# Kernel tuning notes

Measured on AMD Instinct MI355X. Metric: run time of the kernel, lower is better.

The kernel has to match this reference:

```python
import jax, jax.numpy as jnp
import numpy as np

N = 8192
E = 131072
IN_DIM = 3000
HID = 512      # gcn1 out = HID // 2 = 256
OUT = 64
EPS = 1e-12


def gcn_conv(x, W, b, src, dst, n):
    """PyG GCNConv: add self-loops, symmetric norm, gather-matmul-scatter."""
    xw = x @ W                                   # [n, out]
    loop = jnp.arange(n, dtype=src.dtype)
    s = jnp.concatenate([src, loop])             # source j
    d = jnp.concatenate([dst, loop])             # target i
    deg = jax.ops.segment_sum(jnp.ones(s.shape[0], dtype=xw.dtype), d, num_segments=n)
    dinv = deg ** -0.5                           # deg >= 1 due to self-loops
    norm = dinv[s] * dinv[d]                     # [E+n]
    out = jax.ops.segment_sum(norm[:, None] * xw[s], d, num_segments=n)
    return out + b


def avg_readout(emb, mask):
    vsum = mask @ emb                            # [N, h]
    row_sum = jnp.sum(mask, axis=1, keepdims=True)
    g = vsum / row_sum
    nrm = jnp.maximum(jnp.linalg.norm(g, axis=1, keepdims=True), EPS)
    return g / nrm                               # F.normalize(p=2, dim=1)


def bilinear(h, c, Wd, bd):
    # nn.Bilinear(n_h, n_h, 1): out[n,o] = sum_ij h[n,i] Wd[o,i,j] c[n,j] + bd[o]
    return jnp.einsum('ni,oij,nj->no', h, Wd, c) + bd


def setup_inputs() -> dict:
    key = jax.random.key(0)
    k1, k2, k3, k4, k5, k6, k7 = jax.random.split(key, 7)
    gene_data = jax.random.normal(k1, (N, IN_DIM), dtype=jnp.float32)
    # sparse binary neighborhood mask (~16 neighbors/row) + self so row sums > 0
    mask = (jax.random.uniform(k2, (N, N)) < (16.0 / N)).astype(jnp.float32)
    mask = jnp.maximum(mask, jnp.eye(N, dtype=jnp.float32))
    spatial_edge_index = jax.random.randint(k3, (2, E), 0, N, dtype=jnp.int64)
    perm = jax.random.permutation(k4, N).astype(jnp.int64)
    h1 = HID // 2
    W1 = jax.random.normal(k5, (IN_DIM, h1), dtype=jnp.float32) / np.sqrt(IN_DIM)
    b1 = jnp.zeros((h1,), dtype=jnp.float32)
    W2 = jax.random.normal(k6, (h1, OUT), dtype=jnp.float32) / np.sqrt(h1)
    b2 = jnp.zeros((OUT,), dtype=jnp.float32)
    Wd = jax.random.normal(k7, (1, OUT, OUT), dtype=jnp.float32) / np.sqrt(OUT)
    bd = jnp.zeros((1,), dtype=jnp.float32)
    return {"gene_data": gene_data, "mask": mask, "W1": W1, "b1": b1,
            "W2": W2, "b2": b2, "Wd": Wd, "bd": bd,
            "spatial_edge_index": spatial_edge_index, "perm": perm}


def reference(gene_data, mask, W1, b1, W2, b2, Wd, bd, spatial_edge_index, perm):
    src, dst = spatial_edge_index[0], spatial_edge_index[1]
    n = gene_data.shape[0]
    x1 = gene_data
    x1_c = gene_data[perm]                       # permuted (corrupted) graph
    # dropout inactive (eval mode, p=0.0)
    x1 = jax.nn.relu(gcn_conv(x1, W1, b1, src, dst, n))
    x1_c = jax.nn.relu(gcn_conv(x1_c, W1, b1, src, dst, n))
    x1 = jax.nn.relu(gcn_conv(x1, W2, b2, src, dst, n))
    x1_c = jax.nn.relu(gcn_conv(x1_c, W2, b2, src, dst, n))
    g1 = jax.nn.sigmoid(avg_readout(x1, mask))
    g1_c = jax.nn.sigmoid(avg_readout(x1_c, mask))
    ret1 = jnp.concatenate([bilinear(x1, g1, Wd, bd), bilinear(x1_c, g1, Wd, bd)], axis=1)
    ret1_c = jnp.concatenate([bilinear(x1_c, g1_c, Wd, bd), bilinear(x1, g1_c, Wd, bd)], axis=1)
    return (x1, ret1, ret1_c)
```

## Files before the change

### kernel.cpp

```cpp
#include <hip/hip_runtime.h>
#include <hip/hip_bf16.h>

#define NN 8192
#define NMASK 8191
#define IND 3000
#define INDP 3008
#define H1 256
#define OUTD 64

#define GB 512
#define SB 2048
#define PB 544

typedef __bf16 bf16x8 __attribute__((ext_vector_type(8)));
typedef float floatx4 __attribute__((ext_vector_type(4)));

typedef const __attribute__((address_space(1))) void GV;
typedef __attribute__((address_space(3))) void LV;

__device__ __forceinline__ unsigned short f2b(float f) {
    __hip_bfloat16 h = __float2bfloat16(f);
    unsigned short u;
    __builtin_memcpy(&u, &h, 2);
    return u;
}

__device__ __forceinline__ floatx4 b4f(const __hip_bfloat16* p) {
    ushort4 u = *reinterpret_cast<const ushort4*>(p);
    floatx4 r;
    r[0] = __uint_as_float((unsigned)u.x << 16);
    r[1] = __uint_as_float((unsigned)u.y << 16);
    r[2] = __uint_as_float((unsigned)u.z << 16);
    r[3] = __uint_as_float((unsigned)u.w << 16);
    return r;
}


__global__ void k_probe(float code, float* out) {
    if (threadIdx.x == 0 && blockIdx.x == 0) out[0] = code;
}


__global__ void k_pre(const unsigned* __restrict__ eraw, const unsigned* __restrict__ praw,
                      int* __restrict__ flags,
                      const float* __restrict__ W1, const float* __restrict__ W2,
                      __hip_bfloat16* __restrict__ W1t, __hip_bfloat16* __restrict__ W2t) {
    int b = blockIdx.x;
    int t = threadIdx.x;
    if (b < 2) {
        const unsigned* r = (b == 0) ? eraw : praw;
        __shared__ int c;
        if (t == 0) c = 0;
        __syncthreads();
        int z = 0;
        for (int k = t; k < 2048; k += 256)
            if (r[2 * k + 1] == 0u) z++;
        atomicAdd(&c, z);
        __syncthreads();
        if (t == 0) flags[b] = (c > 1024) ? 1 : 0;
    } else if (b < 4) {
        int idx = (b - 2) * 256 + t;
#pragma unroll
        for (int u = 0; u < 4; ++u) {
            int k = idx * 4 + u;
            int c = k >> 3;
            int r = 3000 + (k & 7);
            W1t[(size_t)c * INDP + r] = __float2bfloat16(0.f);
        }
    } else {
        int idx = (b - 4) * 256 + t;
        if (idx < IND * H1) {
            int r = idx / H1, c = idx % H1;
            W1t[(size_t)c * INDP + r] = __float2bfloat16(W1[idx]);
        } else {
            int j = idx - IND * H1;
            if (j < H1 * OUTD) {
                int r = j / OUTD, c = j % OUTD;
                W2t[(size_t)c * H1 + r] = __float2bfloat16(W2[j]);
            }
        }
    }
}


__device__ __forceinline__ void gemm1_body(char* smem, int blk,
                                           const float* __restrict__ A,
                                           const __hip_bfloat16* __restrict__ Bt,
                                           unsigned short* __restrict__ C) {
    unsigned short* As = (unsigned short*)smem;
    unsigned short* Bs = As + 64 * 72;
    int t = threadIdx.x;
    int n0 = (blk & 3) * 64;
    int m0 = (blk >> 2) * 64;
    int lane = t & 63;
    int w = t >> 6;
    int srow = t >> 2;
    int schunk = (t & 3) * 16;
    const float* Arow = A + (size_t)(m0 + srow) * IND + schunk;
    const unsigned short* Brow = (const unsigned short*)Bt + (size_t)(n0 + srow) * INDP + schunk;

    floatx4 acc0 = {0.f, 0.f, 0.f, 0.f}, acc1 = acc0, acc2 = acc0, acc3 = acc0;
    int msub = w * 16;
    int arow = msub + (lane & 15);
    int koff = (lane >> 4) * 8;
    int nlo = lane & 15;

    float4 pa0, pa1, pa2, pa3;
    uint4 pb0, pb1;
    auto load_tile = [&](int k0) {
        float4 z4 = make_float4(0.f, 0.f, 0.f, 0.f);
        uint4 zu = make_uint4(0u, 0u, 0u, 0u);
        pa0 = z4; pa1 = z4; pa2 = z4; pa3 = z4; pb0 = zu; pb1 = zu;
        int kk = k0 + schunk;
        if (kk < IND) {
            const float* ap = Arow + k0;
            pa0 = *reinterpret_cast<const float4*>(ap);
            pa1 = *reinterpret_cast<const float4*>(ap + 4);
            pb0 = *reinterpret_cast<const uint4*>(Brow + k0);
        }
        if (kk + 8 < IND) {
            const float* ap = Arow + k0 + 8;
            pa2 = *reinterpret_cast<const float4*>(ap);
            pa3 = *reinterpret_cast<const float4*>(ap + 4);
            pb1 = *reinterpret_cast<const uint4*>(Brow + k0 + 8);
        }
    };
    load_tile(0);
    for (int k0 = 0; k0 < IND; k0 += 64) {
        uint4 av0, av1, bv0 = pb0, bv1 = pb1;
        {
            unsigned short t8[8] = {f2b(pa0.x), f2b(pa0.y), f2b(pa0.z), f2b(pa0.w),
                                    f2b(pa1.x), f2b(pa1.y), f2b(pa1.z), f2b(pa1.w)};
            __builtin_memcpy(&av0, t8, 16);
        }
        {
            unsigned short t8[8] = {f2b(pa2.x), f2b(pa2.y), f2b(pa2.z), f2b(pa2.w),
                                    f2b(pa3.x), f2b(pa3.y), f2b(pa3.z), f2b(pa3.w)};
            __builtin_memcpy(&av1, t8, 16);
        }
        __syncthreads();
        *reinterpret_cast<uint4*>(&As[srow * 72 + schunk]) = av0;
        *reinterpret_cast<uint4*>(&As[srow * 72 + schunk + 8]) = av1;
        *reinterpret_cast<uint4*>(&Bs[srow * 72 + schunk]) = bv0;
        *reinterpret_cast<uint4*>(&Bs[srow * 72 + schunk + 8]) = bv1;
        __syncthreads();
        if (k0 + 64 < IND) load_tile(k0 + 64);
#pragma unroll
        for (int ks = 0; ks < 64; ks += 32) {
            bf16x8 af = *reinterpret_cast<const bf16x8*>(&As[arow * 72 + ks + koff]);
            bf16x8 b0 = *reinterpret_cast<const bf16x8*>(&Bs[(0 + nlo) * 72 + ks + koff]);
            bf16x8 b1 = *reinterpret_cast<const bf16x8*>(&Bs[(16 + nlo) * 72 + ks + koff]);
            bf16x8 b2 = *reinterpret_cast<const bf16x8*>(&Bs[(32 + nlo) * 72 + ks + koff]);
            bf16x8 b3 = *reinterpret_cast<const bf16x8*>(&Bs[(48 + nlo) * 72 + ks + koff]);
            acc0 = __builtin_amdgcn_mfma_f32_16x16x32_bf16(af, b0, acc0, 0, 0, 0);
            acc1 = __builtin_amdgcn_mfma_f32_16x16x32_bf16(af, b1, acc1, 0, 0, 0);
            acc2 = __builtin_amdgcn_mfma_f32_16x16x32_bf16(af, b2, acc2, 0, 0, 0);
            acc3 = __builtin_amdgcn_mfma_f32_16x16x32_bf16(af, b3, acc3, 0, 0, 0);
        }
    }
    int crow = msub + (lane >> 4) * 4;
    int ccol = lane & 15;
    floatx4 accs[4] = {acc0, acc1, acc2, acc3};
#pragma unroll
    for (int j = 0; j < 4; ++j) {
#pragma unroll
        for (int r = 0; r < 4; ++r) {
            C[(size_t)(m0 + crow + r) * H1 + (n0 + j * 16 + ccol)] = f2b(accs[j][r]);
        }
    }
}

__device__ __forceinline__ void scan_body(char* smem, int blk,
                                          const float* __restrict__ mask,
                                          uint2* __restrict__ ents_g,
                                          float* __restrict__ rsum,
                                          int* __restrict__ rcnt, int n) {
    float (*ring)[4][512] = reinterpret_cast<float (*)[4][512]>(smem);
    int lane = threadIdx.x & 63;
    int w = threadIdx.x >> 6;
    int row = blk * 4 + w;
    const float* mrow = mask + (size_t)row * n;
    uint2* erow = ents_g + ((size_t)row << 6);

    auto issue = [&](int c) {
        int slot = c & 3;
        const float* g0 = mrow + c * 512 + lane * 4;
        __builtin_amdgcn_global_load_lds((GV*)g0, (LV*)&ring[w][slot][0], 16, 0, 0);
        __builtin_amdgcn_global_load_lds((GV*)(g0 + 256), (LV*)&ring[w][slot][256], 16, 0, 0);
    };
    issue(0);
    issue(1);
    issue(2);

    int base = 0;
    float rs = 0.f;
    unsigned long long below = (lane == 63) ? ~0ull >> 1 : (1ull << lane) - 1;
    for (int k = 0; k < 16; ++k) {
        if (k < 13) {
            issue(k + 3);
            asm volatile("s_waitcnt vmcnt(6)" ::: "memory");
        } else if (k == 13) {
            asm volatile("s_waitcnt vmcnt(4)" ::: "memory");
        } else if (k == 14) {
            asm volatile("s_waitcnt vmcnt(2)" ::: "memory");
        } else {
            asm volatile("s_waitcnt vmcnt(0)" ::: "memory");
        }
        int slot = k & 3;
        floatx4 q0 = *reinterpret_cast<floatx4*>(&ring[w][slot][lane * 4]);
        floatx4 q1 = *reinterpret_cast<floatx4*>(&ring[w][slot][256 + lane * 4]);
        int cb = k * 512 + lane * 4;
#pragma unroll
        for (int u = 0; u < 4; ++u) {
            float v = q0[u];
            unsigned long long bal = __ballot(v != 0.f);
            if (v != 0.f) {
                int r = base + __popcll(bal & below);
                if (r < 64) erow[r] = make_uint2((unsigned)(cb + u), __float_as_uint(v));
                rs += v;
            }
            base += __popcll(bal);
        }
#pragma unroll
        for (int u = 0; u < 4; ++u) {
            float v = q1[u];
            unsigned long long bal = __ballot(v != 0.f);
            if (v != 0.f) {
                int r = base + __popcll(bal & below);
                if (r < 64) erow[r] = make_uint2((unsigned)(cb + 256 + u), __float_as_uint(v));
                rs += v;
            }
            base += __popcll(bal);
        }
    }
#pragma unroll
    for (int off = 32; off; off >>= 1) rs += __shfl_xor(rs, off);
    if (lane == 0) {
        rsum[row] = rs;
        rcnt[row] = min(base, 64);
    }
}

__device__ __forceinline__ void prep_body(int idx,
                                          const unsigned* __restrict__ eraw,
                                          const unsigned* __restrict__ praw,
                                          const int* __restrict__ flags,
                                          int* __restrict__ perm32,
                                          int* __restrict__ cnt,
                                          int* __restrict__ adj, int E, int n) {
    if (idx < E) {
        int f = flags[0];
        unsigned s = f ? eraw[2 * (size_t)idx] : eraw[idx];
        unsigned d = f ? eraw[2 * (size_t)(E + idx)] : eraw[E + idx];
        int si = (int)(s & (unsigned)NMASK);
        int di = (int)(d & (unsigned)NMASK);
        int p = atomicAdd(&cnt[di], 1);
        if (p < 64) adj[(di << 6) | p] = si;
    } else {
        int j = idx - E;
        if (j < n) {
            unsigned v = flags[1] ? praw[2 * (size_t)j] : praw[j];
            perm32[j] = (int)(v & (unsigned)NMASK);
        }
    }
}

__global__ __launch_bounds__(256) void k_mega(const float* __restrict__ gene,
                                              const __hip_bfloat16* __restrict__ W1t,
                                              unsigned short* __restrict__ xw1b,
                                              const float* __restrict__ mask,
                                              uint2* __restrict__ ents_g,
                                              float* __restrict__ rsum,
                                              int* __restrict__ rcnt,
                                              const unsigned* __restrict__ eraw,
                                              const unsigned* __restrict__ praw,
                                              const int* __restrict__ flags,
                                              int* __restrict__ perm32,
                                              int* __restrict__ cnt,
                                              int* __restrict__ adj, int E, int n) {
    __shared__ __align__(16) char smem[32768];
    int b = blockIdx.x;
    if (b < GB) {
        gemm1_body(smem, b, gene, W1t, xw1b);
    } else if (b < GB + SB) {
        scan_body(smem, b - GB, mask, ents_g, rsum, rcnt, n);
    } else {
        prep_body((b - GB - SB) * 256 + threadIdx.x, eraw, praw, flags,
                  perm32, cnt, adj, E, n);
    }
}


__global__ __launch_bounds__(256) void k_agg1(const __hip_bfloat16* __restrict__ xw1,
                                              const int* __restrict__ cnt,
                                              const int* __restrict__ adj,
                                              const int* __restrict__ perm,
                                              const float* __restrict__ b1,
                                              __hip_bfloat16* __restrict__ h_all, int n) {
    int lane = threadIdx.x & 63;
    int i = blockIdx.x * 4 + (threadIdx.x >> 6);
    int ci = cnt[i];
    float di = rsqrtf((float)(1 + ci));
    int pi = perm[i];
    float sw = di * di;
    int c4 = lane * 4;
    floatx4 acc = sw * b4f(xw1 + (size_t)i * H1 + c4);
    floatx4 accc = sw * b4f(xw1 + (size_t)pi * H1 + c4);
    int e = min(ci, 64);
    const int* arow = adj + ((size_t)i << 6);
#pragma unroll 4
    for (int t = 0; t < e; ++t) {
        int j = arow[t];
        float wv = di * rsqrtf((float)(1 + cnt[j]));
        int pj = perm[j];
        acc += wv * b4f(xw1 + (size_t)j * H1 + c4);
        accc += wv * b4f(xw1 + (size_t)pj * H1 + c4);
    }
    floatx4 b4 = *reinterpret_cast<const floatx4*>(b1 + c4);
    ushort4 h0, h1;
    h0.x = f2b(fmaxf(acc[0] + b4[0], 0.f));
    h0.y = f2b(fmaxf(acc[1] + b4[1], 0.f));
    h0.z = f2b(fmaxf(acc[2] + b4[2], 0.f));
    h0.w = f2b(fmaxf(acc[3] + b4[3], 0.f));
    h1.x = f2b(fmaxf(accc[0] + b4[0], 0.f));
    h1.y = f2b(fmaxf(accc[1] + b4[1], 0.f));
    h1.z = f2b(fmaxf(accc[2] + b4[2], 0.f));
    h1.w = f2b(fmaxf(accc[3] + b4[3], 0.f));
    *reinterpret_cast<ushort4*>(h_all + (size_t)i * H1 + c4) = h0;
    *reinterpret_cast<ushort4*>(h_all + (size_t)(n + i) * H1 + c4) = h1;
}


__global__ __launch_bounds__(256) void k_gemm2(const __hip_bfloat16* __restrict__ A,
                                               const __hip_bfloat16* __restrict__ Bt,
                                               float* __restrict__ C,
                                               int M, int N, int K) {
    __shared__ __align__(16) unsigned short As[64 * 40];
    __shared__ __align__(16) unsigned short Bs[64 * 40];
    int t = threadIdx.x;
    int m0 = blockIdx.x * 64;
    int n0 = blockIdx.y * 64;
    int lane = t & 63;
    int w = t >> 6;
    int srow = t >> 2;
    int schunk = (t & 3) * 8;
    size_t aoff = (size_t)(m0 + srow) * K + schunk;
    const unsigned short* Brow = (const unsigned short*)Bt + (size_t)(n0 + srow) * K + schunk;

    floatx4 acc0 = {0.f, 0.f, 0.f, 0.f}, acc1 = acc0, acc2 = acc0, acc3 = acc0;
    int msub = w * 16;
    int arow = msub + (lane & 15);
    int koff = (lane >> 4) * 8;
    int nlo = lane & 15;

    uint4 pa = *reinterpret_cast<const uint4*>((const unsigned short*)A + aoff);
    uint4 pb = *reinterpret_cast<const uint4*>(Brow);
    for (int k0 = 0; k0 < K; k0 += 32) {
        uint4 av = pa, bv = pb;
        __syncthreads();
        *reinterpret_cast<uint4*>(&As[srow * 40 + schunk]) = av;
        *reinterpret_cast<uint4*>(&Bs[srow * 40 + schunk]) = bv;
        __syncthreads();
        if (k0 + 32 < K) {
            pa = *reinterpret_cast<const uint4*>((const unsigned short*)A + aoff + k0 + 32);
            pb = *reinterpret_cast<const uint4*>(Brow + k0 + 32);
        }
        bf16x8 af = *reinterpret_cast<const bf16x8*>(&As[arow * 40 + koff]);
        bf16x8 bf0 = *reinterpret_cast<const bf16x8*>(&Bs[(0 + nlo) * 40 + koff]);
        bf16x8 bf1 = *reinterpret_cast<const bf16x8*>(&Bs[(16 + nlo) * 40 + koff]);
        bf16x8 bf2 = *reinterpret_cast<const bf16x8*>(&Bs[(32 + nlo) * 40 + koff]);
        bf16x8 bf3 = *reinterpret_cast<const bf16x8*>(&Bs[(48 + nlo) * 40 + koff]);
        acc0 = __builtin_amdgcn_mfma_f32_16x16x32_bf16(af, bf0, acc0, 0, 0, 0);
        acc1 = __builtin_amdgcn_mfma_f32_16x16x32_bf16(af, bf1, acc1, 0, 0, 0);
        acc2 = __builtin_amdgcn_mfma_f32_16x16x32_bf16(af, bf2, acc2, 0, 0, 0);
        acc3 = __builtin_amdgcn_mfma_f32_16x16x32_bf16(af, bf3, acc3, 0, 0, 0);
    }
    int crow = msub + (lane >> 4) * 4;
    int ccol = lane & 15;
    floatx4 accs[4] = {acc0, acc1, acc2, acc3};
#pragma unroll
    for (int j = 0; j < 4; ++j) {
#pragma unroll
        for (int r = 0; r < 4; ++r) {
            C[(size_t)(m0 + crow + r) * N + (n0 + j * 16 + ccol)] = accs[j][r];
        }
    }
}


__global__ __launch_bounds__(256) void k_agg2(const float* __restrict__ hw_all,
                                              const int* __restrict__ cnt,
                                              const int* __restrict__ adj,
                                              const float* __restrict__ b2,
                                              float* __restrict__ x1_all,
                                              float* __restrict__ out_x1, int n) {
    int lane = threadIdx.x & 63;
    int i = blockIdx.x * 4 + (threadIdx.x >> 6);
    int ci = cnt[i];
    float di = rsqrtf((float)(1 + ci));
    float sw = di * di;
    float acc = sw * hw_all[(size_t)i * OUTD + lane];
    float accc = sw * hw_all[(size_t)(n + i) * OUTD + lane];
    int e = min(ci, 64);
    const int* arow = adj + ((size_t)i << 6);
#pragma unroll 4
    for (int t = 0; t < e; ++t) {
        int j = arow[t];
        float wv = di * rsqrtf((float)(1 + cnt[j]));
        acc += wv * hw_all[(size_t)j * OUTD + lane];
        accc += wv * hw_all[(size_t)(n + j) * OUTD + lane];
    }
    float b = b2[lane];
    float v = fmaxf(acc + b, 0.f);
    float vc = fmaxf(accc + b, 0.f);
    x1_all[(size_t)i * OUTD + lane] = v;
    x1_all[(size_t)(n + i) * OUTD + lane] = vc;
    out_x1[(size_t)i * OUTD + lane] = v;
}


__global__ __launch_bounds__(256) void k_finish(const float* __restrict__ x1_all,
                                                const uint2* __restrict__ ents_g,
                                                const float* __restrict__ rsum,
                                                const int* __restrict__ rcnt,
                                                const float* __restrict__ Wd,
                                                const float* __restrict__ bd,
                                                float* __restrict__ ret1,
                                                float* __restrict__ ret1c, int n) {
    int lane = threadIdx.x & 63;
    int w = threadIdx.x >> 6;
    int row = blockIdx.x * 4 + w;
    int cnt = rcnt[row];
    float rs = rsum[row];
    const uint2* erow = ents_g + ((size_t)row << 6);
    float acc = 0.f, accc = 0.f;
#pragma unroll 2
    for (int e = 0; e < cnt; ++e) {
        uint2 ent = erow[e];
        float m = __uint_as_float(ent.y);
        int j = (int)ent.x;
        acc += m * x1_all[(size_t)j * OUTD + lane];
        accc += m * x1_all[(size_t)(n + j) * OUTD + lane];
    }
    float rst = fmaxf(rs, 1e-20f);
    float g = acc / rst;
    float gc = accc / rst;
    float s1 = g * g, s2 = gc * gc;
#pragma unroll
    for (int off = 32; off; off >>= 1) {
        s1 += __shfl_xor(s1, off);
        s2 += __shfl_xor(s2, off);
    }
    float gn = g / fmaxf(sqrtf(s1), 1e-12f);
    float gnc = gc / fmaxf(sqrtf(s2), 1e-12f);
    float gsig = 1.f / (1.f + __expf(-gn));
    float gcsig = 1.f / (1.f + __expf(-gnc));
    float tg = 0.f, tgc = 0.f;
    const float* wrow = Wd + lane * 64;
#pragma unroll 8
    for (int j = 0; j < 64; ++j) {
        float gj = __shfl(gsig, j);
        float gcj = __shfl(gcsig, j);
        float wv = wrow[j];
        tg += wv * gj;
        tgc += wv * gcj;
    }
    float x = x1_all[(size_t)row * OUTD + lane];
    float xc = x1_all[(size_t)(n + row) * OUTD + lane];
    float r0 = x * tg, r1 = xc * tg, r2 = xc * tgc, r3 = x * tgc;
#pragma unroll
    for (int off = 32; off; off >>= 1) {
        r0 += __shfl_down(r0, off);
        r1 += __shfl_down(r1, off);
        r2 += __shfl_down(r2, off);
        r3 += __shfl_down(r3, off);
    }
    if (lane == 0) {
        float b = bd[0];
        ret1[(size_t)row * 2 + 0] = r0 + b;
        ret1[(size_t)row * 2 + 1] = r1 + b;
        ret1c[(size_t)row * 2 + 0] = r2 + b;
        ret1c[(size_t)row * 2 + 1] = r3 + b;
    }
}


extern "C" void kernel_launch(void* const* d_in, const int* in_sizes, int n_in,
                              void* d_out, int out_size, void* d_ws, size_t ws_size,
                              hipStream_t stream) {
    const float* gene = (const float*)d_in[0];
    const float* mask = (const float*)d_in[1];
    const float* W1 = (const float*)d_in[2];
    const float* b1 = (const float*)d_in[3];
    const float* W2 = (const float*)d_in[4];
    const float* b2 = (const float*)d_in[5];
    const float* Wd = (const float*)d_in[6];
    const float* bd = (const float*)d_in[7];
    const unsigned* eidx_raw = (const unsigned*)d_in[8];
    const unsigned* perm_raw = (const unsigned*)d_in[9];
    const int n = NN;
    const int E = in_sizes[8] / 2;

    char* base = (char*)d_ws;
    char* p = base;
    auto alloc = [&](size_t bytes) -> char* {
        char* r = p;
        p += (bytes + 255) & ~(size_t)255;
        return r;
    };
    int* flags = (int*)alloc(256);
    int* cnt = (int*)alloc((size_t)n * 4);
    int* adj = (int*)alloc((size_t)n * 64 * 4);
    int* perm32 = (int*)alloc((size_t)n * 4);
    uint2* ents_g = (uint2*)alloc((size_t)n * 64 * 8);
    float* rsum = (float*)alloc((size_t)n * 4);
    int* rcnt = (int*)alloc((size_t)n * 4);
    __hip_bfloat16* W2t = (__hip_bfloat16*)alloc((size_t)H1 * OUTD * 2);
    __hip_bfloat16* W1t = (__hip_bfloat16*)alloc((size_t)INDP * H1 * 2);
    __hip_bfloat16* xw1b = (__hip_bfloat16*)alloc((size_t)n * H1 * 2);
    __hip_bfloat16* h_all = (__hip_bfloat16*)alloc((size_t)2 * n * H1 * 2);
    size_t need = (size_t)(p - base);
    float* hw_all = (float*)xw1b;
    float* x1_all = (float*)h_all;

    float* out_x1 = (float*)d_out;
    float* out_ret1 = out_x1 + (size_t)n * OUTD;
    float* out_ret1c = out_ret1 + (size_t)n * 2;

    if (ws_size < need) {
        k_probe<<<1, 64, 0, stream>>>(1000.f + (float)(ws_size >> 20), out_x1);
        return;
    }

    hipMemsetAsync(cnt, 0, (size_t)n * 4, stream);

    k_pre<<<4 + (IND * H1 + H1 * OUTD + 255) / 256, 256, 0, stream>>>(
        eidx_raw, perm_raw, flags, W1, W2, W1t, W2t);

    k_mega<<<GB + SB + PB, 256, 0, stream>>>(gene, W1t, (unsigned short*)xw1b,
                                             mask, ents_g, rsum, rcnt,
                                             eidx_raw, perm_raw, flags,
                                             perm32, cnt, adj, E, n);

    k_agg1<<<n / 4, 256, 0, stream>>>(xw1b, cnt, adj, perm32, b1, h_all, n);

    k_gemm2<<<dim3(2 * n / 64, OUTD / 64), 256, 0, stream>>>(h_all, W2t, hw_all, 2 * n, OUTD, H1);

    k_agg2<<<n / 4, 256, 0, stream>>>(hw_all, cnt, adj, b2, x1_all, out_x1, n);

    k_finish<<<n / 4, 256, 0, stream>>>(x1_all, ents_g, rsum, rcnt, Wd, bd,
                                        out_ret1, out_ret1c, n);
}
```

Baseline: 545.4 us.

## Scan mask with grid-strided chunks and atomic compaction instead of per-row LDS ring

The mask scan no longer assigns one full row to each wave streamed through an LDS ring via global_load_lds. Each wave now processes 16 grid-strided 512-element chunks, loaded straight into registers with a two-deep register prefetch. Nonzeros go into a small per-wave LDS buffer and are then scattered to per-row entry lists using atomic slot counters, and row sums are also built with atomics. rcnt and rsum sit next to cnt so a single memset clears all three. This spreads the memory traffic more evenly and cuts LDS use, at the cost of atomics and nondeterministic entry order. A wave silently drops any nonzeros beyond 56, which is safe only while the mask stays sparse.

```diff
diff --git a/kernel.cpp b/kernel.cpp
--- a/kernel.cpp
+++ b/kernel.cpp
@@ -11,12 +11,10 @@
 #define GB 512
 #define SB 2048
 #define PB 544
+#define SW (SB * 4)
 
 typedef __bf16 bf16x8 __attribute__((ext_vector_type(8)));
 typedef float floatx4 __attribute__((ext_vector_type(4)));
-
-typedef const __attribute__((address_space(1))) void GV;
-typedef __attribute__((address_space(3))) void LV;
 
 __device__ __forceinline__ unsigned short f2b(float f) {
     __hip_bfloat16 h = __float2bfloat16(f);
@@ -175,69 +173,55 @@
                                           uint2* __restrict__ ents_g,
                                           float* __restrict__ rsum,
                                           int* __restrict__ rcnt, int n) {
-    float (*ring)[4][512] = reinterpret_cast<float (*)[4][512]>(smem);
+    uint2 (*ebuf)[56] = reinterpret_cast<uint2 (*)[56]>(smem);
     int lane = threadIdx.x & 63;
     int w = threadIdx.x >> 6;
-    int row = blk * 4 + w;
-    const float* mrow = mask + (size_t)row * n;
-    uint2* erow = ents_g + ((size_t)row << 6);
-
-    auto issue = [&](int c) {
-        int slot = c & 3;
-        const float* g0 = mrow + c * 512 + lane * 4;
-        __builtin_amdgcn_global_load_lds((GV*)g0, (LV*)&ring[w][slot][0], 16, 0, 0);
-        __builtin_amdgcn_global_load_lds((GV*)(g0 + 256), (LV*)&ring[w][slot][256], 16, 0, 0);
+    int gw = blk * 4 + w;
+    unsigned long long below = (lane == 63) ? ~0ull >> 1 : (1ull << lane) - 1;
+
+    auto cptr = [&](int t) {
+        return mask + (((size_t)(gw + t * SW)) << 9) + lane * 8;
     };
-    issue(0);
-    issue(1);
-    issue(2);
+    floatx4 pa0 = *reinterpret_cast<const floatx4*>(cptr(0));
+    floatx4 pa1 = *reinterpret_cast<const floatx4*>(cptr(0) + 4);
+    floatx4 pb0 = *reinterpret_cast<const floatx4*>(cptr(1));
+    floatx4 pb1 = *reinterpret_cast<const floatx4*>(cptr(1) + 4);
 
     int base = 0;
-    float rs = 0.f;
-    unsigned long long below = (lane == 63) ? ~0ull >> 1 : (1ull << lane) - 1;
-    for (int k = 0; k < 16; ++k) {
-        if (k < 13) {
-            issue(k + 3);
-            asm volatile("s_waitcnt vmcnt(6)" ::: "memory");
-        } else if (k == 13) {
-            asm volatile("s_waitcnt vmcnt(4)" ::: "memory");
-        } else if (k == 14) {
-            asm volatile("s_waitcnt vmcnt(2)" ::: "memory");
-        } else {
-            asm volatile("s_waitcnt vmcnt(0)" ::: "memory");
-        }
-        int slot = k & 3;
-        floatx4 q0 = *reinterpret_cast<floatx4*>(&ring[w][slot][lane * 4]);
-        floatx4 q1 = *reinterpret_cast<floatx4*>(&ring[w][slot][256 + lane * 4]);
-        int cb = k * 512 + lane * 4;
-#pragma unroll
-        for (int u = 0; u < 4; ++u) {
-            float v = q0[u];
+    for (int t = 0; t < 16; ++t) {
+        floatx4 c0 = pa0, c1 = pa1;
+        pa0 = pb0; pa1 = pb1;
+        if (t + 2 < 16) {
+            pb0 = *reinterpret_cast<const floatx4*>(cptr(t + 2));
+            pb1 = *reinterpret_cast<const floatx4*>(cptr(t + 2) + 4);
+        }
+        int c = gw + t * SW;
+        int row = c >> 4;
+        int cb = (c & 15) * 512 + lane * 8;
+        float lsum = 0.f;
+        float va[8] = {c0[0], c0[1], c0[2], c0[3], c1[0], c1[1], c1[2], c1[3]};
+#pragma unroll
+        for (int u = 0; u < 8; ++u) {
+            float v = va[u];
             unsigned long long bal = __ballot(v != 0.f);
             if (v != 0.f) {
                 int r = base + __popcll(bal & below);
-                if (r < 64) erow[r] = make_uint2((unsigned)(cb + u), __float_as_uint(v));
-                rs += v;
+                if (r < 56)
+                    ebuf[w][r] = make_uint2(((unsigned)row << 13) | (unsigned)(cb + u),
+                                            __float_as_uint(v));
+                lsum += v;
             }
             base += __popcll(bal);
         }
-#pragma unroll
-        for (int u = 0; u < 4; ++u) {
-            float v = q1[u];
-            unsigned long long bal = __ballot(v != 0.f);
-            if (v != 0.f) {
-                int r = base + __popcll(bal & below);
-                if (r < 64) erow[r] = make_uint2((unsigned)(cb + 256 + u), __float_as_uint(v));
-                rs += v;
-            }
-            base += __popcll(bal);
-        }
-    }
-#pragma unroll
-    for (int off = 32; off; off >>= 1) rs += __shfl_xor(rs, off);
-    if (lane == 0) {
-        rsum[row] = rs;
-        rcnt[row] = min(base, 64);
+        if (lsum != 0.f) atomicAdd(&rsum[row], lsum);
+    }
+    int tot = min(base, 56);
+    if (lane < tot) {
+        uint2 e = ebuf[w][lane];
+        int row = (int)(e.x >> 13);
+        int slot = atomicAdd(&rcnt[row], 1);
+        if (slot < 64)
+            ents_g[((size_t)row << 6) | slot] = make_uint2(e.x & 8191u, e.y);
     }
 }
 
@@ -278,7 +262,7 @@
                                               int* __restrict__ perm32,
                                               int* __restrict__ cnt,
                                               int* __restrict__ adj, int E, int n) {
-    __shared__ __align__(16) char smem[32768];
+    __shared__ __align__(16) char smem[18432];
     int b = blockIdx.x;
     if (b < GB) {
         gemm1_body(smem, b, gene, W1t, xw1b);
@@ -430,7 +414,7 @@
     int lane = threadIdx.x & 63;
     int w = threadIdx.x >> 6;
     int row = blockIdx.x * 4 + w;
-    int cnt = rcnt[row];
+    int cnt = min(rcnt[row], 64);
     float rs = rsum[row];
     const uint2* erow = ents_g + ((size_t)row << 6);
     float acc = 0.f, accc = 0.f;
@@ -510,11 +494,11 @@
     };
     int* flags = (int*)alloc(256);
     int* cnt = (int*)alloc((size_t)n * 4);
+    int* rcnt = (int*)alloc((size_t)n * 4);
+    float* rsum = (float*)alloc((size_t)n * 4);
     int* adj = (int*)alloc((size_t)n * 64 * 4);
     int* perm32 = (int*)alloc((size_t)n * 4);
     uint2* ents_g = (uint2*)alloc((size_t)n * 64 * 8);
-    float* rsum = (float*)alloc((size_t)n * 4);
-    int* rcnt = (int*)alloc((size_t)n * 4);
     __hip_bfloat16* W2t = (__hip_bfloat16*)alloc((size_t)H1 * OUTD * 2);
     __hip_bfloat16* W1t = (__hip_bfloat16*)alloc((size_t)INDP * H1 * 2);
     __hip_bfloat16* xw1b = (__hip_bfloat16*)alloc((size_t)n * H1 * 2);
@@ -532,7 +516,7 @@
         return;
     }
 
-    hipMemsetAsync(cnt, 0, (size_t)n * 4, stream);
+    hipMemsetAsync(cnt, 0, (size_t)3 * n * 4, stream);
 
     k_pre<<<4 + (IND * H1 + H1 * OUTD + 255) / 256, 256, 0, stream>>>(
         eidx_raw, perm_raw, flags, W1, W2, W1t, W2t);
```

New measurement: 553.2 us. About the same (+1.4%).
